# Performance work log

Measured on AMD Instinct MI355X. Metric: run time of the kernel, lower is better.

The kernel has to match this reference:

```python
import jax, jax.numpy as jnp
import numpy as np

N = 8192
IN_DIM = 512
OUT_DIM = 256
ALPHA = 0.2  # LeakyReLU negative slope


def setup_inputs() -> dict:
    key = jax.random.key(0)
    k_nodes, k_edge, k_W, k_Wb, k_a1, k_a1b, k_a2, k_a2b = jax.random.split(key, 8)
    nodes = jax.random.normal(k_nodes, (N, IN_DIM), dtype=jnp.float32)
    edge_mat = jax.random.uniform(k_edge, (N, N)) > 0.5
    edge_mat = edge_mat | jnp.eye(N, dtype=bool)
    s_W = 1.0 / np.sqrt(IN_DIM)
    s_a = 1.0 / np.sqrt(OUT_DIM)
    W_w = jax.random.uniform(k_W, (OUT_DIM, IN_DIM), minval=-s_W, maxval=s_W, dtype=jnp.float32)
    W_b = jax.random.uniform(k_Wb, (OUT_DIM,), minval=-s_W, maxval=s_W, dtype=jnp.float32)
    a1_w = jax.random.uniform(k_a1, (1, OUT_DIM), minval=-s_a, maxval=s_a, dtype=jnp.float32)
    a1_b = jax.random.uniform(k_a1b, (1,), minval=-s_a, maxval=s_a, dtype=jnp.float32)
    a2_w = jax.random.uniform(k_a2, (1, OUT_DIM), minval=-s_a, maxval=s_a, dtype=jnp.float32)
    a2_b = jax.random.uniform(k_a2b, (1,), minval=-s_a, maxval=s_a, dtype=jnp.float32)
    return {"nodes": nodes, "edge_mat": edge_mat, "W_w": W_w, "W_b": W_b,
            "a1_w": a1_w, "a1_b": a1_b, "a2_w": a2_w, "a2_b": a2_b}


def reference(nodes, edge_mat, W_w, W_b, a1_w, a1_b, a2_w, a2_b):
    Wh = nodes @ W_w.T + W_b                      # [N, OUT_DIM]
    Wh1 = Wh @ a1_w.T + a1_b                      # [N, 1]
    Wh2 = Wh @ a2_w.T + a2_b                      # [N, 1]
    scores = jax.nn.leaky_relu(Wh1 + Wh2.T, negative_slope=ALPHA)  # [N, N]
    masked = jnp.where(edge_mat, scores, -jnp.inf)
    attention = jax.nn.softmax(masked, axis=1)    # [N, N]
    return attention @ Wh                         # [N, OUT_DIM]
```

## Files before the change

### kernel.cpp

```cpp
#include <hip/hip_runtime.h>
#include <hip/hip_bf16.h>
#include <stdint.h>


#define NN 8192
#define IND 512
#define OUTD 256

typedef __attribute__((ext_vector_type(8))) short short8;
typedef __attribute__((ext_vector_type(4))) short short4v;
typedef __attribute__((ext_vector_type(4))) float f32x4;

static __device__ __forceinline__ short f2bf(float f) {
  return __builtin_bit_cast(short, __float2bfloat16(f));
}

extern "C" __global__ __launch_bounds__(256) void k_convert_w(
    const float* __restrict__ W, short* __restrict__ W2) {
  const int t = blockIdx.x * 256 + threadIdx.x;
  const int row = t >> 6, kb = t & 63;
  const float* src = W + row * IND + kb * 8;
  f32x4 x0 = *(const f32x4*)src;
  f32x4 x1 = *(const f32x4*)(src + 4);
  short8 o;
  o[0] = f2bf(x0[0]); o[1] = f2bf(x0[1]); o[2] = f2bf(x0[2]); o[3] = f2bf(x0[3]);
  o[4] = f2bf(x1[0]); o[5] = f2bf(x1[1]); o[6] = f2bf(x1[2]); o[7] = f2bf(x1[3]);
  *(short8*)(W2 + (size_t)kb * 2048 + row * 8) = o;
}

extern "C" __global__ __launch_bounds__(128) void k_wh(
    const float* __restrict__ nodes, const short* __restrict__ W2,
    const float* __restrict__ Wb, const float* __restrict__ a1w,
    const float* __restrict__ a1b, const float* __restrict__ a2w,
    const float* __restrict__ a2b, short* __restrict__ WhL,
    float* __restrict__ s1, float* __restrict__ s2) {
  const int tid = threadIdx.x;
  const int wv = tid >> 6, lane = tid & 63, g = lane >> 4, m = lane & 15;
  const int rowbase = blockIdx.x * 32 + wv * 16;

  f32x4 acc[16];
#pragma unroll
  for (int nf = 0; nf < 16; ++nf) acc[nf] = (f32x4){0.f, 0.f, 0.f, 0.f};

  const float* arow = nodes + (size_t)(rowbase + m) * IND;
  const short* bb = W2 + (size_t)g * 2048 + m * 8;
#pragma unroll 4
  for (int k0 = 0; k0 < IND; k0 += 32) {
    const float* ap = arow + k0 + g * 8;
    f32x4 x0 = *(const f32x4*)ap;
    f32x4 x1 = *(const f32x4*)(ap + 4);
    short8 af;
    af[0] = f2bf(x0[0]); af[1] = f2bf(x0[1]); af[2] = f2bf(x0[2]); af[3] = f2bf(x0[3]);
    af[4] = f2bf(x1[0]); af[5] = f2bf(x1[1]); af[6] = f2bf(x1[2]); af[7] = f2bf(x1[3]);
    const short* bk = bb + (size_t)(k0 >> 3) * 2048;
#pragma unroll
    for (int nf = 0; nf < 16; ++nf) {
      short8 bf = *(const short8*)(bk + nf * 128);
      acc[nf] = __builtin_amdgcn_mfma_f32_16x16x32_bf16(af, bf, acc[nf], 0, 0, 0);
    }
  }

  float p1[4] = {0.f, 0.f, 0.f, 0.f}, p2[4] = {0.f, 0.f, 0.f, 0.f};
#pragma unroll
  for (int nf = 0; nf < 16; ++nf) {
    const int n = nf * 16 + m;
    const float b = Wb[n], c1 = a1w[n], c2 = a2w[n];
#pragma unroll
    for (int r = 0; r < 4; ++r) {
      float v = acc[nf][r] + b;
      acc[nf][r] = v;
      p1[r] += c1 * v;
      p2[r] += c2 * v;
    }
  }
#pragma unroll
  for (int off = 1; off < 16; off <<= 1) {
#pragma unroll
    for (int r = 0; r < 4; ++r) {
      p1[r] += __shfl_xor(p1[r], off);
      p2[r] += __shfl_xor(p2[r], off);
    }
  }
  if (m == 0) {
    const float b1 = a1b[0], b2 = a2b[0];
#pragma unroll
    for (int r = 0; r < 4; ++r) {
      const int row = rowbase + g * 4 + r;
      s1[row] = p1[r] + b1;
      s2[row] = p2[r] + b2;
    }
  }

  const size_t cbase = ((size_t)(rowbase >> 3) + (g >> 1)) * 2048 + (g & 1) * 4;
#pragma unroll
  for (int nf = 0; nf < 16; ++nf) {
    short4v o;
#pragma unroll
    for (int r = 0; r < 4; ++r) o[r] = f2bf(acc[nf][r]);
    *(short4v*)(WhL + cbase + (size_t)(nf * 16 + m) * 8) = o;
  }
}

extern "C" __global__ __launch_bounds__(256) void k_mask(
    const int* __restrict__ mask, uint32_t* __restrict__ bm) {
  const int tid = threadIdx.x;
  const int wv = tid >> 6, lane = tid & 63;
  const int gw = blockIdx.x * 4 + wv;
  const size_t base = (size_t)gw * 16384;
#pragma unroll 4
  for (int it = 0; it < 64; ++it) {
    const size_t ib = base + (size_t)it * 256;
    unsigned long long b0 = __ballot(mask[ib + lane] != 0);
    unsigned long long b1 = __ballot(mask[ib + 64 + lane] != 0);
    unsigned long long b2 = __ballot(mask[ib + 128 + lane] != 0);
    unsigned long long b3 = __ballot(mask[ib + 192 + lane] != 0);
    if (lane < 8) {
      unsigned long long s01 = (lane & 2) ? b1 : b0;
      unsigned long long s23 = (lane & 2) ? b3 : b2;
      unsigned long long sel = (lane & 4) ? s23 : s01;
      bm[ib / 32 + lane] = (uint32_t)(sel >> ((lane & 1) * 32));
    }
  }
}

extern "C" __global__ __launch_bounds__(512, 4) void k_attn(
    const uint32_t* __restrict__ bm, const short* __restrict__ WhL,
    const float* __restrict__ s1, const float* __restrict__ s2,
    float* __restrict__ pnum, float* __restrict__ pden) {
  __shared__ short Bs[2][8192];

  const int tid = threadIdx.x;
  const int w = tid >> 6, lane = tid & 63, g = lane >> 4, m = lane & 15;
  const int rt = blockIdx.x >> 3, jc = blockIdx.x & 7;
  const int rg = w & 3, ns = w >> 2;
  const int rb = rt * 128 + rg * 32;

  const float s1a = s1[rb + m];
  const float s1b = s1[rb + 16 + m];

  f32x4 acc0[8], acc1[8];
#pragma unroll
  for (int nf = 0; nf < 8; ++nf) {
    acc0[nf] = (f32x4){0.f, 0.f, 0.f, 0.f};
    acc1[nf] = (f32x4){0.f, 0.f, 0.f, 0.f};
  }
  float den0 = 0.f, den1 = 0.f;

  const uint32_t* bw0 = bm + (size_t)(rb + m) * 256 + jc * 32;
  const float* sp = s2 + jc * 1024 + g * 8;
  const short* gW = WhL + (size_t)jc * 128 * 2048 + tid * 8;

  auto build = [&](float s1h, uint32_t bits, const f32x4& slo, const f32x4& shi,
                   float& den) -> short8 {
    short8 af;
#pragma unroll
    for (int i = 0; i < 8; ++i) {
      float sv = s1h + (i < 4 ? slo[i] : shi[i - 4]);
      sv = fmaxf(sv, 0.2f * sv);
      float pv = (bits & (1u << i)) ? __expf(sv) : 0.f;
      den += pv;
      af[i] = f2bf(pv);
    }
    return af;
  };

  short8 sg0 = *(const short8*)(gW);
  short8 sg1 = *(const short8*)(gW + 4096);
  uint32_t cw0 = bw0[0], cw1 = bw0[16 * 256];
  *(short8*)(&Bs[0][tid * 8]) = sg0;
  *(short8*)(&Bs[0][4096 + tid * 8]) = sg1;
  __syncthreads();

  for (int u = 0; u < 32; ++u) {
    if (u < 31) {
      sg0 = *(const short8*)(gW + (size_t)(u + 1) * 8192);
      sg1 = *(const short8*)(gW + (size_t)(u + 1) * 8192 + 4096);
    }
    const int un = (u < 31) ? u + 1 : 31;
    const uint32_t nw0 = bw0[un], nw1 = bw0[16 * 256 + un];

    const f32x4 cs0 = *(const f32x4*)(sp + u * 32);
    const f32x4 cs1 = *(const f32x4*)(sp + u * 32 + 4);
    short8 af0 = build(s1a, cw0 >> (g * 8), cs0, cs1, den0);
    short8 af1 = build(s1b, cw1 >> (g * 8), cs0, cs1, den1);
    const short* bl = &Bs[u & 1][g * 2048 + (ns * 128 + m) * 8];
#pragma unroll
    for (int nf = 0; nf < 8; ++nf) {
      short8 bf = *(const short8*)(bl + nf * 128);
      acc0[nf] = __builtin_amdgcn_mfma_f32_16x16x32_bf16(af0, bf, acc0[nf], 0, 0, 0);
      acc1[nf] = __builtin_amdgcn_mfma_f32_16x16x32_bf16(af1, bf, acc1[nf], 0, 0, 0);
    }
    if (u < 31) {
      *(short8*)(&Bs[(u + 1) & 1][tid * 8]) = sg0;
      *(short8*)(&Bs[(u + 1) & 1][4096 + tid * 8]) = sg1;
    }
    cw0 = nw0; cw1 = nw1;
    __syncthreads();
  }

  den0 += __shfl_xor(den0, 16); den0 += __shfl_xor(den0, 32);
  den1 += __shfl_xor(den1, 16); den1 += __shfl_xor(den1, 32);
  if (ns == 0 && lane < 16) {
    pden[jc * NN + rb + m] = den0;
    pden[jc * NN + rb + 16 + m] = den1;
  }

  float* pn = pnum + (size_t)jc * NN * OUTD + (size_t)rb * OUTD + ns * 128;
#pragma unroll
  for (int r = 0; r < 4; ++r) {
    const int q = g * 4 + r;
#pragma unroll
    for (int nf = 0; nf < 8; ++nf) {
      pn[(size_t)q * OUTD + nf * 16 + m] = acc0[nf][r];
      pn[(size_t)(16 + q) * OUTD + nf * 16 + m] = acc1[nf][r];
    }
  }
}

extern "C" __global__ __launch_bounds__(256) void k_comb(
    const float* __restrict__ pnum, const float* __restrict__ pden,
    float* __restrict__ out) {
  const int idx = blockIdx.x * 256 + threadIdx.x;
  const int row = idx >> 6, c4 = (idx & 63) * 4;
  f32x4 s = (f32x4){0.f, 0.f, 0.f, 0.f};
  float d = 0.f;
#pragma unroll
  for (int jc = 0; jc < 8; ++jc) {
    f32x4 v = *(const f32x4*)(pnum + ((size_t)jc * NN + row) * OUTD + c4);
    s += v;
    d += pden[jc * NN + row];
  }
  const float inv = 1.f / d;
  *(f32x4*)(out + (size_t)row * OUTD + c4) = s * inv;
}

extern "C" void kernel_launch(void* const* d_in, const int* in_sizes, int n_in,
                              void* d_out, int out_size, void* d_ws, size_t ws_size,
                              hipStream_t stream) {
  const float* nodes = (const float*)d_in[0];
  const int*   mask  = (const int*)d_in[1];
  const float* W_w   = (const float*)d_in[2];
  const float* W_b   = (const float*)d_in[3];
  const float* a1w   = (const float*)d_in[4];
  const float* a1b   = (const float*)d_in[5];
  const float* a2w   = (const float*)d_in[6];
  const float* a2b   = (const float*)d_in[7];
  float* out = (float*)d_out;

  char* ws = (char*)d_ws;
  short*    WhL  = (short*)(ws);
  float*    s1   = (float*)(ws + (size_t)4  * 1024 * 1024);
  float*    s2   = (float*)(ws + (size_t)4  * 1024 * 1024 + 32768);
  short*    W2   = (short*)(ws + (size_t)4  * 1024 * 1024 + 65536);
  uint32_t* bmp  = (uint32_t*)(ws + (size_t)5  * 1024 * 1024);
  float*    pnum = (float*)(ws + (size_t)16 * 1024 * 1024);
  float*    pden = (float*)(ws + (size_t)96 * 1024 * 1024);

  hipLaunchKernelGGL(k_convert_w, dim3(64), dim3(256), 0, stream, W_w, W2);
  hipLaunchKernelGGL(k_wh, dim3(256), dim3(128), 0, stream,
                     nodes, W2, W_b, a1w, a1b, a2w, a2b, WhL, s1, s2);
  hipLaunchKernelGGL(k_mask, dim3(1024), dim3(256), 0, stream, mask, bmp);
  hipLaunchKernelGGL(k_attn, dim3(512), dim3(512), 0, stream,
                     bmp, WhL, s1, s2, pnum, pden);
  hipLaunchKernelGGL(k_comb, dim3(2048), dim3(256), 0, stream,
                     pnum, pden, out);
}
```

Baseline: 191.7 us.

## Use direct global-to-LDS loads for Wh tiles and halve attention block size

```diff
diff --git a/kernel.cpp b/kernel.cpp
--- a/kernel.cpp
+++ b/kernel.cpp
@@ -10,6 +10,9 @@
 typedef __attribute__((ext_vector_type(8))) short short8;
 typedef __attribute__((ext_vector_type(4))) short short4v;
 typedef __attribute__((ext_vector_type(4))) float f32x4;
+
+#define AS_GLOBAL __attribute__((address_space(1)))
+#define AS_LDS __attribute__((address_space(3)))
 
 static __device__ __forceinline__ short f2bf(float f) {
   return __builtin_bit_cast(short, __float2bfloat16(f));
@@ -123,7 +126,7 @@
   }
 }
 
-extern "C" __global__ __launch_bounds__(512, 4) void k_attn(
+extern "C" __global__ __launch_bounds__(256, 4) void k_attn(
     const uint32_t* __restrict__ bm, const short* __restrict__ WhL,
     const float* __restrict__ s1, const float* __restrict__ s2,
     float* __restrict__ pnum, float* __restrict__ pden) {
@@ -132,8 +135,8 @@
   const int tid = threadIdx.x;
   const int w = tid >> 6, lane = tid & 63, g = lane >> 4, m = lane & 15;
   const int rt = blockIdx.x >> 3, jc = blockIdx.x & 7;
-  const int rg = w & 3, ns = w >> 2;
-  const int rb = rt * 128 + rg * 32;
+  const int rg = w & 1, ns = w >> 1;
+  const int rb = rt * 64 + rg * 32;
 
   const float s1a = s1[rb + m];
   const float s1b = s1[rb + 16 + m];
@@ -147,8 +150,9 @@
   float den0 = 0.f, den1 = 0.f;
 
   const uint32_t* bw0 = bm + (size_t)(rb + m) * 256 + jc * 32;
+  const uint32_t* bw1 = bw0 + (size_t)16 * 256;
   const float* sp = s2 + jc * 1024 + g * 8;
-  const short* gW = WhL + (size_t)jc * 128 * 2048 + tid * 8;
+  const short* gWu = WhL + (size_t)jc * 262144 + w * 2048 + lane * 8;
 
   auto build = [&](float s1h, uint32_t bits, const f32x4& slo, const f32x4& shi,
                    float& den) -> short8 {
@@ -164,20 +168,28 @@
     return af;
   };
 
-  short8 sg0 = *(const short8*)(gW);
-  short8 sg1 = *(const short8*)(gW + 4096);
-  uint32_t cw0 = bw0[0], cw1 = bw0[16 * 256];
-  *(short8*)(&Bs[0][tid * 8]) = sg0;
-  *(short8*)(&Bs[0][4096 + tid * 8]) = sg1;
+#pragma unroll
+  for (int c = 0; c < 4; ++c) {
+    __builtin_amdgcn_global_load_lds(
+        (const AS_GLOBAL void*)(gWu + c * 512),
+        (AS_LDS void*)(&Bs[0][w * 2048 + c * 512]), 16, 0, 0);
+  }
+  uint32_t cw0 = bw0[0], cw1 = bw1[0];
   __syncthreads();
 
   for (int u = 0; u < 32; ++u) {
     if (u < 31) {
-      sg0 = *(const short8*)(gW + (size_t)(u + 1) * 8192);
-      sg1 = *(const short8*)(gW + (size_t)(u + 1) * 8192 + 4096);
+      const short* gn = gWu + (size_t)(u + 1) * 8192;
+      short* ld = &Bs[(u + 1) & 1][w * 2048];
+#pragma unroll
+      for (int c = 0; c < 4; ++c) {
+        __builtin_amdgcn_global_load_lds(
+            (const AS_GLOBAL void*)(gn + c * 512),
+            (AS_LDS void*)(ld + c * 512), 16, 0, 0);
+      }
     }
     const int un = (u < 31) ? u + 1 : 31;
-    const uint32_t nw0 = bw0[un], nw1 = bw0[16 * 256 + un];
+    const uint32_t nw0 = bw0[un], nw1 = bw1[un];
 
     const f32x4 cs0 = *(const f32x4*)(sp + u * 32);
     const f32x4 cs1 = *(const f32x4*)(sp + u * 32 + 4);
@@ -189,10 +201,6 @@
       short8 bf = *(const short8*)(bl + nf * 128);
       acc0[nf] = __builtin_amdgcn_mfma_f32_16x16x32_bf16(af0, bf, acc0[nf], 0, 0, 0);
       acc1[nf] = __builtin_amdgcn_mfma_f32_16x16x32_bf16(af1, bf, acc1[nf], 0, 0, 0);
-    }
-    if (u < 31) {
-      *(short8*)(&Bs[(u + 1) & 1][tid * 8]) = sg0;
-      *(short8*)(&Bs[(u + 1) & 1][4096 + tid * 8]) = sg1;
     }
     cw0 = nw0; cw1 = nw1;
     __syncthreads();
@@ -260,7 +268,7 @@
   hipLaunchKernelGGL(k_wh, dim3(256), dim3(128), 0, stream,
                      nodes, W2, W_b, a1w, a1b, a2w, a2b, WhL, s1, s2);
   hipLaunchKernelGGL(k_mask, dim3(1024), dim3(256), 0, stream, mask, bmp);
-  hipLaunchKernelGGL(k_attn, dim3(512), dim3(512), 0, stream,
+  hipLaunchKernelGGL(k_attn, dim3(1024), dim3(256), 0, stream,
                      bmp, WhL, s1, s2, pnum, pden);
   hipLaunchKernelGGL(k_comb, dim3(2048), dim3(256), 0, stream,
                      pnum, pden, out);
```

Measured after the change: 185.5 us. 3.2% less time.
